# Kernel optimization log

Measured on AMD Instinct MI355X. Metric: run time of the kernel, lower is better.

The kernel has to match this reference:

```python
import jax, jax.numpy as jnp
import numpy as np

SMOOTH = 1e-5
ALPHA = 0.25
GAMMA = 2.0
INIT_BETA = 0.5
BETA_DECAY = 0.99


def setup_inputs() -> dict:
    key = jax.random.key(0)
    ks = jax.random.split(key, 7)
    B, NC, C, H, W, D = 8, 1000, 19, 512, 512, 768
    return {
        "logits": jax.random.normal(ks[0], (B, NC), dtype=jnp.float32),
        "label": jax.random.randint(ks[1], (B,), 0, NC),
        "vision_feat": jax.random.normal(ks[2], (B, D), dtype=jnp.float32),
        "text_feat": jax.random.normal(ks[3], (B, D), dtype=jnp.float32),
        "modal_mask": jax.random.uniform(ks[4], (B, 2), dtype=jnp.float32),
        "seg_mask": jax.random.normal(ks[5], (B, C, H, W), dtype=jnp.float32),
        "seg_gt": jax.random.randint(ks[6], (B, H, W), 0, C),
        "epoch": 5,
    }


def _ce_mean(logits, label):
    logp = jax.nn.log_softmax(logits, axis=-1)
    return -jnp.take_along_axis(logp, label[:, None], axis=-1).mean()


def _dice_loss(pred, target):
    # pred: [B,C,H,W] (raw, as in the torch module), target: [B,H,W] int
    C = pred.shape[1]
    onehot = (target[:, None, :, :] == jnp.arange(C)[None, :, None, None]).astype(pred.dtype)
    inter = jnp.sum(pred * onehot, axis=(2, 3))          # [B,C]
    union = jnp.sum(pred, axis=(2, 3)) + jnp.sum(onehot, axis=(2, 3))
    dice = (2.0 * inter + SMOOTH) / (union + SMOOTH)
    return jnp.mean(1.0 - dice)


def _focal_loss(pred, target):
    # pred: [B,C,H,W] logits over class axis 1
    logp = jax.nn.log_softmax(pred, axis=1)
    logp_t = jnp.take_along_axis(logp, target[:, None, :, :], axis=1)[:, 0]  # [B,H,W]
    p_t = jnp.exp(logp_t)
    ce = -logp_t
    return jnp.mean(ALPHA * (1.0 - p_t) ** GAMMA * ce)


def _modal_balance(vision_feat, text_feat, modal_mask, epoch):
    beta_t = INIT_BETA * BETA_DECAY ** epoch
    vn = vision_feat / jnp.linalg.norm(vision_feat, axis=1, keepdims=True)
    tn = text_feat / jnp.linalg.norm(text_feat, axis=1, keepdims=True)
    v_cons = jnp.mean((vn - vn.mean(axis=0, keepdims=True)) ** 2)
    t_cons = jnp.mean((tn - tn.mean(axis=0, keepdims=True)) ** 2)
    cross = 1.0 - jnp.mean(jnp.sum(vn * tn, axis=1))  # cosine sim of unit vectors
    return ((1.0 - beta_t) * v_cons * modal_mask[:, 0].mean()
            + beta_t * t_cons * modal_mask[:, 1].mean() + cross)


def reference(logits, label, vision_feat, text_feat, modal_mask, seg_mask, seg_gt, epoch):
    ce = _ce_mean(logits, label)
    mb = _modal_balance(vision_feat, text_feat, modal_mask, epoch)
    seg = _dice_loss(seg_mask, seg_gt) + _focal_loss(seg_mask, seg_gt)
    total = ce + 0.3 * mb + 0.5 * seg
    return total
```

## Files before the change

### kernel.cpp

```cpp
#include <hip/hip_runtime.h>
#include <math.h>

#define SMOOTH_F 1e-5f
#define ALPHA_F 0.25f

constexpr int Bn = 8;
constexpr int NCn = 1000;
constexpr int Cn = 19;
constexpr int HWn = 512 * 512;
constexpr int Dn = 768;
constexpr int BC = Bn * Cn;

constexpr int TPB = 256;
constexpr int CHUNK = 2048;
constexpr int CHUNKS_PER_B = HWn / CHUNK;
constexpr int SEG_BLOCKS = Bn * CHUNKS_PER_B;
constexpr int GROUPS = CHUNK / (TPB * 4);

constexpr int WS_INTER = 0;
constexpr int WS_PRED  = BC;
constexpr int WS_CNT   = 2 * BC;
constexpr int WS_FOCAL = 3 * BC;
constexpr int WS_CE    = 3 * BC + 1;
constexpr int WS_MB    = 3 * BC + 2;
constexpr int WS_N     = 3 * BC + 3;

__device__ __forceinline__ float wave_sum(float v) {
#pragma unroll
  for (int off = 32; off > 0; off >>= 1) v += __shfl_down(v, off, 64);
  return v;
}
__device__ __forceinline__ float wave_max(float v) {
#pragma unroll
  for (int off = 32; off > 0; off >>= 1) v = fmaxf(v, __shfl_down(v, off, 64));
  return v;
}

__global__ __launch_bounds__(256) void k_zero(float* __restrict__ ws) {
  int t = blockIdx.x * blockDim.x + threadIdx.x;
  if (t < WS_N) ws[t] = 0.0f;
}

__global__ __launch_bounds__(256) void k_small(
    const float* __restrict__ logits, const int* __restrict__ label,
    const float* __restrict__ vf, const float* __restrict__ tf,
    const float* __restrict__ mmask, const int* __restrict__ epoch,
    float* __restrict__ ws) {
  __shared__ float sA[4];
  __shared__ float sBv[4];
  __shared__ float nv[Bn];
  __shared__ float nt[Bn];
  __shared__ float s3[3][4];
  const int tid = threadIdx.x;
  const int wid = tid >> 6, lane = tid & 63;

  if (blockIdx.x == 0) {
    float acc = 0.0f;
    for (int b = 0; b < Bn; ++b) {
      const float* row = logits + b * NCn;
      float lm = -INFINITY;
      for (int j = tid; j < NCn; j += TPB) lm = fmaxf(lm, row[j]);
      lm = wave_max(lm);
      if (lane == 0) sA[wid] = lm;
      __syncthreads();
      float bm = fmaxf(fmaxf(sA[0], sA[1]), fmaxf(sA[2], sA[3]));
      __syncthreads();
      float ls = 0.0f;
      for (int j = tid; j < NCn; j += TPB) ls += expf(row[j] - bm);
      ls = wave_sum(ls);
      if (lane == 0) sA[wid] = ls;
      __syncthreads();
      if (tid == 0) {
        float lse = bm + logf(sA[0] + sA[1] + sA[2] + sA[3]);
        acc += row[label[b]] - lse;
      }
      __syncthreads();
    }
    if (tid == 0) ws[WS_CE] = -(acc / (float)Bn);
  } else {
    for (int b = 0; b < Bn; ++b) {
      float sv = 0.0f, st = 0.0f;
      for (int j = tid; j < Dn; j += TPB) {
        float a = vf[b * Dn + j];
        float c = tf[b * Dn + j];
        sv += a * a;
        st += c * c;
      }
      sv = wave_sum(sv);
      st = wave_sum(st);
      if (lane == 0) { sA[wid] = sv; sBv[wid] = st; }
      __syncthreads();
      if (tid == 0) {
        nv[b] = sqrtf(sA[0] + sA[1] + sA[2] + sA[3]);
        nt[b] = sqrtf(sBv[0] + sBv[1] + sBv[2] + sBv[3]);
      }
      __syncthreads();
    }
    float colv = 0.0f, colt = 0.0f, cross = 0.0f;
    for (int j = tid; j < Dn; j += TPB) {
      float sv = 0.0f, ssv = 0.0f, stt = 0.0f, sst = 0.0f, cr = 0.0f;
      for (int b = 0; b < Bn; ++b) {
        float vn = vf[b * Dn + j] / nv[b];
        float tn = tf[b * Dn + j] / nt[b];
        sv += vn; ssv += vn * vn;
        stt += tn; sst += tn * tn;
        cr += vn * tn;
      }
      colv += ssv - sv * sv * 0.125f;
      colt += sst - stt * stt * 0.125f;
      cross += cr;
    }
    colv = wave_sum(colv);
    colt = wave_sum(colt);
    cross = wave_sum(cross);
    if (lane == 0) { s3[0][wid] = colv; s3[1][wid] = colt; s3[2][wid] = cross; }
    __syncthreads();
    if (tid == 0) {
      float cv = s3[0][0] + s3[0][1] + s3[0][2] + s3[0][3];
      float ct = s3[1][0] + s3[1][1] + s3[1][2] + s3[1][3];
      float cr = s3[2][0] + s3[2][1] + s3[2][2] + s3[2][3];
      float v_cons = cv / (float)(Bn * Dn);
      float t_cons = ct / (float)(Bn * Dn);
      float crossv = 1.0f - cr * 0.125f;
      float beta = 0.5f * powf(0.99f, (float)epoch[0]);
      float mm0 = 0.0f, mm1 = 0.0f;
      for (int b = 0; b < Bn; ++b) { mm0 += mmask[b * 2]; mm1 += mmask[b * 2 + 1]; }
      mm0 *= 0.125f; mm1 *= 0.125f;
      ws[WS_MB] = (1.0f - beta) * v_cons * mm0 + beta * t_cons * mm1 + crossv;
    }
  }
}

__global__ __launch_bounds__(TPB) void k_seg(
    const float* __restrict__ pred, const int* __restrict__ gt,
    float* __restrict__ ws) {
  __shared__ float s_inter[Cn];
  __shared__ float s_count[Cn];
  __shared__ float s_pred[Cn];
  __shared__ float s_red[4];

  const int tid = threadIdx.x;
  const int wid = tid >> 6, lane = tid & 63;
  const int b = blockIdx.x / CHUNKS_PER_B;
  const int chunk = blockIdx.x % CHUNKS_PER_B;

  if (tid < Cn) { s_inter[tid] = 0.0f; s_count[tid] = 0.0f; s_pred[tid] = 0.0f; }
  __syncthreads();

  const float4* predb = (const float4*)(pred + (size_t)b * Cn * HWn);
  const int4* gtb = (const int4*)(gt + (size_t)b * HWn);
  const int base4 = chunk * (CHUNK / 4);

  float psum[Cn];
#pragma unroll
  for (int c = 0; c < Cn; ++c) psum[c] = 0.0f;
  float focal = 0.0f;

#pragma unroll 1
  for (int g = 0; g < GROUPS; ++g) {
    const int idx4 = base4 + g * TPB + tid;
    const int4 t4 = gtb[idx4];
    float4 xs[Cn];
#pragma unroll
    for (int c = 0; c < Cn; ++c)
      xs[c] = predb[(size_t)c * (HWn / 4) + idx4];

    float4 m = xs[0];
#pragma unroll
    for (int c = 1; c < Cn; ++c) {
      m.x = fmaxf(m.x, xs[c].x); m.y = fmaxf(m.y, xs[c].y);
      m.z = fmaxf(m.z, xs[c].z); m.w = fmaxf(m.w, xs[c].w);
    }
    float4 se = make_float4(0.f, 0.f, 0.f, 0.f);
    float4 xt = make_float4(0.f, 0.f, 0.f, 0.f);
#pragma unroll
    for (int c = 0; c < Cn; ++c) {
      se.x += expf(xs[c].x - m.x); se.y += expf(xs[c].y - m.y);
      se.z += expf(xs[c].z - m.z); se.w += expf(xs[c].w - m.w);
      if (t4.x == c) xt.x = xs[c].x;
      if (t4.y == c) xt.y = xs[c].y;
      if (t4.z == c) xt.z = xs[c].z;
      if (t4.w == c) xt.w = xs[c].w;
      psum[c] += (xs[c].x + xs[c].y) + (xs[c].z + xs[c].w);
    }
    float4 lse;
    lse.x = m.x + logf(se.x); lse.y = m.y + logf(se.y);
    lse.z = m.z + logf(se.z); lse.w = m.w + logf(se.w);

    {
      float lpt, p, om;
      lpt = xt.x - lse.x; p = expf(lpt); om = 1.0f - p; focal += om * om * (-lpt);
      lpt = xt.y - lse.y; p = expf(lpt); om = 1.0f - p; focal += om * om * (-lpt);
      lpt = xt.z - lse.z; p = expf(lpt); om = 1.0f - p; focal += om * om * (-lpt);
      lpt = xt.w - lse.w; p = expf(lpt); om = 1.0f - p; focal += om * om * (-lpt);
    }
    atomicAdd(&s_inter[t4.x], xt.x);
    atomicAdd(&s_inter[t4.y], xt.y);
    atomicAdd(&s_inter[t4.z], xt.z);
    atomicAdd(&s_inter[t4.w], xt.w);
    atomicAdd(&s_count[t4.x], 1.0f);
    atomicAdd(&s_count[t4.y], 1.0f);
    atomicAdd(&s_count[t4.z], 1.0f);
    atomicAdd(&s_count[t4.w], 1.0f);
  }

  focal *= ALPHA_F;
  float fw = wave_sum(focal);
  if (lane == 0) s_red[wid] = fw;
#pragma unroll
  for (int c = 0; c < Cn; ++c) {
    float v = wave_sum(psum[c]);
    if (lane == 0) atomicAdd(&s_pred[c], v);
  }
  __syncthreads();

  if (tid < Cn) {
    atomicAdd(&ws[WS_INTER + b * Cn + tid], s_inter[tid]);
    atomicAdd(&ws[WS_PRED + b * Cn + tid], s_pred[tid]);
    atomicAdd(&ws[WS_CNT + b * Cn + tid], s_count[tid]);
  }
  if (tid == 0)
    atomicAdd(&ws[WS_FOCAL], s_red[0] + s_red[1] + s_red[2] + s_red[3]);
}

__global__ __launch_bounds__(256) void k_final(
    const float* __restrict__ ws, float* __restrict__ out) {
  __shared__ float sA[4];
  const int tid = threadIdx.x;
  const int wid = tid >> 6, lane = tid & 63;
  float v = 0.0f;
  if (tid < BC) {
    float inter = ws[WS_INTER + tid];
    float ps = ws[WS_PRED + tid];
    float cnt = ws[WS_CNT + tid];
    float dice = (2.0f * inter + SMOOTH_F) / (ps + cnt + SMOOTH_F);
    v = 1.0f - dice;
  }
  v = wave_sum(v);
  if (lane == 0) sA[wid] = v;
  __syncthreads();
  if (tid == 0) {
    float dice_mean = (sA[0] + sA[1] + sA[2] + sA[3]) / (float)BC;
    float focal_mean = ws[WS_FOCAL] / (float)(Bn * HWn);
    float seg = dice_mean + focal_mean;
    out[0] = ws[WS_CE] + 0.3f * ws[WS_MB] + 0.5f * seg;
  }
}

extern "C" void kernel_launch(void* const* d_in, const int* in_sizes, int n_in,
                              void* d_out, int out_size, void* d_ws, size_t ws_size,
                              hipStream_t stream) {
  const float* logits = (const float*)d_in[0];
  const int* label    = (const int*)d_in[1];
  const float* vf     = (const float*)d_in[2];
  const float* tf     = (const float*)d_in[3];
  const float* mmask  = (const float*)d_in[4];
  const float* seg    = (const float*)d_in[5];
  const int* gt       = (const int*)d_in[6];
  const int* epoch    = (const int*)d_in[7];
  float* out = (float*)d_out;
  float* ws = (float*)d_ws;

  hipLaunchKernelGGL(k_zero, dim3(2), dim3(256), 0, stream, ws);
  hipLaunchKernelGGL(k_small, dim3(2), dim3(256), 0, stream,
                     logits, label, vf, tf, mmask, epoch, ws);
  hipLaunchKernelGGL(k_seg, dim3(SEG_BLOCKS), dim3(TPB), 0, stream, seg, gt, ws);
  hipLaunchKernelGGL(k_final, dim3(1), dim3(256), 0, stream, ws, out);
}
```

Before: 286.1 us.

## Stage segmentation chunks through LDS with smaller per-block tiles and merge zeroing kernel

The segmentation kernel now uses 512-pixel chunks instead of 2048, giving four times as many blocks. Each block copies its 19-class tile into shared memory with coalesced float4 loads, then each thread processes two pixels from LDS in one pass instead of looping. The aim is more memory-level parallelism and fewer stalls on the large per-thread register load set. The workspace-zeroing kernel is folded into the small-loss kernel as an extra block, removing one launch. In exchange there are four times more global atomics and per-block reductions, and about 38 KB of LDS per block, which caps occupancy.

```diff
diff --git a/kernel.cpp b/kernel.cpp
--- a/kernel.cpp
+++ b/kernel.cpp
@@ -12,10 +12,11 @@
 constexpr int BC = Bn * Cn;
 
 constexpr int TPB = 256;
-constexpr int CHUNK = 2048;
-constexpr int CHUNKS_PER_B = HWn / CHUNK;
-constexpr int SEG_BLOCKS = Bn * CHUNKS_PER_B;
-constexpr int GROUPS = CHUNK / (TPB * 4);
+constexpr int CHUNK = 512;
+constexpr int CPB = HWn / CHUNK;
+constexpr int SEG_BLOCKS = Bn * CPB;
+constexpr int F4_PER_CLASS = CHUNK / 4;
+constexpr int LDS_F4 = Cn * F4_PER_CLASS;
 
 constexpr int WS_INTER = 0;
 constexpr int WS_PRED  = BC;
@@ -23,7 +24,7 @@
 constexpr int WS_FOCAL = 3 * BC;
 constexpr int WS_CE    = 3 * BC + 1;
 constexpr int WS_MB    = 3 * BC + 2;
-constexpr int WS_N     = 3 * BC + 3;
+constexpr int WS_ZERO_N = WS_FOCAL + 1;
 
 __device__ __forceinline__ float wave_sum(float v) {
 #pragma unroll
@@ -36,12 +37,7 @@
   return v;
 }
 
-__global__ __launch_bounds__(256) void k_zero(float* __restrict__ ws) {
-  int t = blockIdx.x * blockDim.x + threadIdx.x;
-  if (t < WS_N) ws[t] = 0.0f;
-}
-
-__global__ __launch_bounds__(256) void k_small(
+__global__ __launch_bounds__(256) void k_pre(
     const float* __restrict__ logits, const int* __restrict__ label,
     const float* __restrict__ vf, const float* __restrict__ tf,
     const float* __restrict__ mmask, const int* __restrict__ epoch,
@@ -55,6 +51,8 @@
   const int wid = tid >> 6, lane = tid & 63;
 
   if (blockIdx.x == 0) {
+    for (int t = tid; t < WS_ZERO_N; t += TPB) ws[t] = 0.0f;
+  } else if (blockIdx.x == 1) {
     float acc = 0.0f;
     for (int b = 0; b < Bn; ++b) {
       const float* row = logits + b * NCn;
@@ -134,6 +132,7 @@
 __global__ __launch_bounds__(TPB) void k_seg(
     const float* __restrict__ pred, const int* __restrict__ gt,
     float* __restrict__ ws) {
+  __shared__ float lds[Cn * CHUNK];
   __shared__ float s_inter[Cn];
   __shared__ float s_count[Cn];
   __shared__ float s_pred[Cn];
@@ -141,75 +140,64 @@
 
   const int tid = threadIdx.x;
   const int wid = tid >> 6, lane = tid & 63;
-  const int b = blockIdx.x / CHUNKS_PER_B;
-  const int chunk = blockIdx.x % CHUNKS_PER_B;
+  const int b = blockIdx.x / CPB;
+  const int chunk = blockIdx.x % CPB;
 
   if (tid < Cn) { s_inter[tid] = 0.0f; s_count[tid] = 0.0f; s_pred[tid] = 0.0f; }
+
+  const float4* pred4 = (const float4*)pred;
+  float4* lds4 = (float4*)lds;
+  const size_t pbase = (size_t)b * Cn * (HWn / 4) + (size_t)chunk * F4_PER_CLASS;
+  for (int i = tid; i < LDS_F4; i += TPB) {
+    const int c = i >> 7;
+    const int off = i & 127;
+    lds4[i] = pred4[pbase + (size_t)c * (HWn / 4) + off];
+  }
+  const int2 t2 = ((const int2*)(gt + (size_t)b * HWn))[chunk * (CHUNK / 2) + tid];
   __syncthreads();
 
-  const float4* predb = (const float4*)(pred + (size_t)b * Cn * HWn);
-  const int4* gtb = (const int4*)(gt + (size_t)b * HWn);
-  const int base4 = chunk * (CHUNK / 4);
-
+  const float2* lds2 = (const float2*)lds;
+  float2 xs[Cn];
+#pragma unroll
+  for (int c = 0; c < Cn; ++c) xs[c] = lds2[c * (CHUNK / 2) + tid];
+
+  float m0 = xs[0].x, m1 = xs[0].y;
+#pragma unroll
+  for (int c = 1; c < Cn; ++c) {
+    m0 = fmaxf(m0, xs[c].x);
+    m1 = fmaxf(m1, xs[c].y);
+  }
+  float se0 = 0.0f, se1 = 0.0f, xt0 = 0.0f, xt1 = 0.0f;
   float psum[Cn];
 #pragma unroll
-  for (int c = 0; c < Cn; ++c) psum[c] = 0.0f;
-  float focal = 0.0f;
-
-#pragma unroll 1
-  for (int g = 0; g < GROUPS; ++g) {
-    const int idx4 = base4 + g * TPB + tid;
-    const int4 t4 = gtb[idx4];
-    float4 xs[Cn];
-#pragma unroll
-    for (int c = 0; c < Cn; ++c)
-      xs[c] = predb[(size_t)c * (HWn / 4) + idx4];
-
-    float4 m = xs[0];
-#pragma unroll
-    for (int c = 1; c < Cn; ++c) {
-      m.x = fmaxf(m.x, xs[c].x); m.y = fmaxf(m.y, xs[c].y);
-      m.z = fmaxf(m.z, xs[c].z); m.w = fmaxf(m.w, xs[c].w);
-    }
-    float4 se = make_float4(0.f, 0.f, 0.f, 0.f);
-    float4 xt = make_float4(0.f, 0.f, 0.f, 0.f);
-#pragma unroll
-    for (int c = 0; c < Cn; ++c) {
-      se.x += expf(xs[c].x - m.x); se.y += expf(xs[c].y - m.y);
-      se.z += expf(xs[c].z - m.z); se.w += expf(xs[c].w - m.w);
-      if (t4.x == c) xt.x = xs[c].x;
-      if (t4.y == c) xt.y = xs[c].y;
-      if (t4.z == c) xt.z = xs[c].z;
-      if (t4.w == c) xt.w = xs[c].w;
-      psum[c] += (xs[c].x + xs[c].y) + (xs[c].z + xs[c].w);
-    }
-    float4 lse;
-    lse.x = m.x + logf(se.x); lse.y = m.y + logf(se.y);
-    lse.z = m.z + logf(se.z); lse.w = m.w + logf(se.w);
-
-    {
-      float lpt, p, om;
-      lpt = xt.x - lse.x; p = expf(lpt); om = 1.0f - p; focal += om * om * (-lpt);
-      lpt = xt.y - lse.y; p = expf(lpt); om = 1.0f - p; focal += om * om * (-lpt);
-      lpt = xt.z - lse.z; p = expf(lpt); om = 1.0f - p; focal += om * om * (-lpt);
-      lpt = xt.w - lse.w; p = expf(lpt); om = 1.0f - p; focal += om * om * (-lpt);
-    }
-    atomicAdd(&s_inter[t4.x], xt.x);
-    atomicAdd(&s_inter[t4.y], xt.y);
-    atomicAdd(&s_inter[t4.z], xt.z);
-    atomicAdd(&s_inter[t4.w], xt.w);
-    atomicAdd(&s_count[t4.x], 1.0f);
-    atomicAdd(&s_count[t4.y], 1.0f);
-    atomicAdd(&s_count[t4.z], 1.0f);
-    atomicAdd(&s_count[t4.w], 1.0f);
-  }
-
+  for (int c = 0; c < Cn; ++c) {
+    se0 += expf(xs[c].x - m0);
+    se1 += expf(xs[c].y - m1);
+    if (t2.x == c) xt0 = xs[c].x;
+    if (t2.y == c) xt1 = xs[c].y;
+    psum[c] = xs[c].x + xs[c].y;
+  }
+  const float lse0 = m0 + logf(se0);
+  const float lse1 = m1 + logf(se1);
+
+  float focal;
+  {
+    float lpt, p, om;
+    lpt = xt0 - lse0; p = expf(lpt); om = 1.0f - p; focal = om * om * (-lpt);
+    lpt = xt1 - lse1; p = expf(lpt); om = 1.0f - p; focal += om * om * (-lpt);
+  }
   focal *= ALPHA_F;
-  float fw = wave_sum(focal);
+
+  atomicAdd(&s_inter[t2.x], xt0);
+  atomicAdd(&s_inter[t2.y], xt1);
+  atomicAdd(&s_count[t2.x], 1.0f);
+  atomicAdd(&s_count[t2.y], 1.0f);
+
+  const float fw = wave_sum(focal);
   if (lane == 0) s_red[wid] = fw;
 #pragma unroll
   for (int c = 0; c < Cn; ++c) {
-    float v = wave_sum(psum[c]);
+    const float v = wave_sum(psum[c]);
     if (lane == 0) atomicAdd(&s_pred[c], v);
   }
   __syncthreads();
@@ -230,19 +218,19 @@
   const int wid = tid >> 6, lane = tid & 63;
   float v = 0.0f;
   if (tid < BC) {
-    float inter = ws[WS_INTER + tid];
-    float ps = ws[WS_PRED + tid];
-    float cnt = ws[WS_CNT + tid];
-    float dice = (2.0f * inter + SMOOTH_F) / (ps + cnt + SMOOTH_F);
+    const float inter = ws[WS_INTER + tid];
+    const float ps = ws[WS_PRED + tid];
+    const float cnt = ws[WS_CNT + tid];
+    const float dice = (2.0f * inter + SMOOTH_F) / (ps + cnt + SMOOTH_F);
     v = 1.0f - dice;
   }
   v = wave_sum(v);
   if (lane == 0) sA[wid] = v;
   __syncthreads();
   if (tid == 0) {
-    float dice_mean = (sA[0] + sA[1] + sA[2] + sA[3]) / (float)BC;
-    float focal_mean = ws[WS_FOCAL] / (float)(Bn * HWn);
-    float seg = dice_mean + focal_mean;
+    const float dice_mean = (sA[0] + sA[1] + sA[2] + sA[3]) / (float)BC;
+    const float focal_mean = ws[WS_FOCAL] / (float)(Bn * HWn);
+    const float seg = dice_mean + focal_mean;
     out[0] = ws[WS_CE] + 0.3f * ws[WS_MB] + 0.5f * seg;
   }
 }
@@ -261,8 +249,7 @@
   float* out = (float*)d_out;
   float* ws = (float*)d_ws;
 
-  hipLaunchKernelGGL(k_zero, dim3(2), dim3(256), 0, stream, ws);
-  hipLaunchKernelGGL(k_small, dim3(2), dim3(256), 0, stream,
+  hipLaunchKernelGGL(k_pre, dim3(3), dim3(256), 0, stream,
                      logits, label, vf, tf, mmask, epoch, ws);
   hipLaunchKernelGGL(k_seg, dim3(SEG_BLOCKS), dim3(TPB), 0, stream, seg, gt, ws);
   hipLaunchKernelGGL(k_final, dim3(1), dim3(256), 0, stream, ws, out);
```

After: 325.7 us. 1.14x slower.
